# Kernel optimization log

Hardware: AMD Instinct MI355X
Metric: run time of the kernel (lower is better)

## Reference

```python
import jax, jax.numpy as jnp
import numpy as np

ECNUM = 100
CA1NUM = 100
CA3NUM = 100
ACTNUM = 2
TRACKLEN = 100
SIGMA = 5.0
BS = 4096


def setup_inputs() -> dict:
    key = jax.random.key(0)
    ks = jax.random.split(key, 10)
    cue_train = jax.random.randint(ks[0], (BS, TRACKLEN), 0, 3).astype(jnp.int32) - 1  # values in {-1,0,1}
    ec3_last = jax.random.uniform(ks[1], (BS, ECNUM), dtype=jnp.float32)
    ec5_last = jax.random.uniform(ks[2], (BS, ECNUM), dtype=jnp.float32)
    ca1_last = jnp.zeros((BS, CA1NUM), dtype=jnp.float32)
    cueL = (jax.random.uniform(ks[3], (ECNUM,)) < 0.2).astype(jnp.float32)
    cueR = (jax.random.uniform(ks[4], (ECNUM,)) < 0.2).astype(jnp.float32)
    Wec3ca1 = 0.01 * jax.random.uniform(ks[5], (ECNUM, CA1NUM), dtype=jnp.float32)
    Wca3ca1 = 0.01 * jax.random.uniform(ks[6], (CA3NUM, CA1NUM), dtype=jnp.float32)
    Wca1ec5 = 0.01 * jax.random.normal(ks[7], (CA1NUM, ECNUM), dtype=jnp.float32)
    Wca1act = 0.01 * jax.random.uniform(ks[8], (CA1NUM, ACTNUM), dtype=jnp.float32)
    ca1bias = 0.01 * jax.random.uniform(ks[9], (CA1NUM,), dtype=jnp.float32)
    return {
        "bs": BS,
        "cue_train": cue_train,
        "ec3_last": ec3_last,
        "ec5_last": ec5_last,
        "ca1_last": ca1_last,
        "cueL": cueL,
        "cueR": cueR,
        "Wec3ca1": Wec3ca1,
        "Wca3ca1": Wca3ca1,
        "Wca1ec5": Wca1ec5,
        "Wca1act": Wca1act,
        "ca1bias": ca1bias,
    }


def reference(bs, cue_train, ec3_last, ec5_last, ca1_last, cueL, cueR,
              Wec3ca1, Wca3ca1, Wca1ec5, Wca1act, ca1bias):
    # Precompute position-dependent CA3 activity for every timestep: [T, ca3num]
    centers = jnp.linspace(0.0, float(TRACKLEN), CA3NUM)
    xs = jnp.arange(TRACKLEN, dtype=jnp.float32)
    ca3_all = jnp.exp(-(((xs[:, None] - centers[None, :]) / SIGMA) ** 2) / 2.0)
    drive = ca3_all @ Wca3ca1  # [T, ca1num]

    # Sensory input per timestep via conditional gather: [T, bs, ecnum]
    cue_t = cue_train.T[:, :, None]  # [T, bs, 1]
    sensory = jnp.where(cue_t == 1, cueL[None, None, :],
                        jnp.where(cue_t == -1, cueR[None, None, :], 0.0))

    def step(carry, inp):
        ec3, ec5 = carry
        d, s = inp  # d: [ca1num], s: [bs, ecnum]
        ca1 = jax.nn.relu(d[None, :] * (1.0 + jax.nn.sigmoid(ec3 @ Wec3ca1)) - ca1bias)
        ec5 = ec5 + ca1 @ Wca1ec5
        ec5 = 0.69 + 0.3 * jax.nn.sigmoid(4.0 * (ec5 - 0.3))
        ec3 = ec5 * ec3 + s
        return (ec3, ec5), ca1

    (ec3, ec5), ca1his = jax.lax.scan(step, (ec3_last, ec5_last), (drive, sensory))
    ca1 = ca1his[-1]
    actCell = ca1 @ Wca1act
    return actCell, ca1his, ec3, ec5, ca1
```

## Files before the change

### kernel.cpp

```cpp
#include <hip/hip_runtime.h>

#define TLEN 100
#define ECN  100
#define CA1N 100
#define CA3N 100
#define BSZ  4096
#define ACTN 2
#define BT   16

typedef short bf16x8 __attribute__((ext_vector_type(8)));
typedef float f32x4  __attribute__((ext_vector_type(4)));

__device__ __forceinline__ unsigned short f2bf(float f){
  union { float f; unsigned int u; } c; c.f = f;
  return (unsigned short)((c.u + 0x8000u) >> 16);
}
__device__ __forceinline__ float fsigm(float x){
  float e = __expf(-x);
  return __builtin_amdgcn_rcpf(1.0f + e);
}

__global__ void drive_kernel(const float* __restrict__ Wca3ca1, float* __restrict__ drive){
  __shared__ float ca3row[CA3N];
  const int t = blockIdx.x, tid = threadIdx.x;
  if (tid < CA3N){
    float c = (float)tid * (100.0f / 99.0f);
    float d = ((float)t - c) * 0.2f;
    ca3row[tid] = __expf(-0.5f * d * d);
  }
  __syncthreads();
  if (tid < CA1N){
    float acc = 0.f;
    for (int k = 0; k < CA3N; ++k) acc = fmaf(ca3row[k], Wca3ca1[k*CA1N + tid], acc);
    drive[t*CA1N + tid] = acc;
  }
}


__global__ __launch_bounds__(512, 2)
void rnn_kernel(const int*   __restrict__ cue_train,
                const float* __restrict__ ec3_last,
                const float* __restrict__ ec5_last,
                const float* __restrict__ cueL,
                const float* __restrict__ cueR,
                const float* __restrict__ Wec3ca1,
                const float* __restrict__ Wca1ec5,
                const float* __restrict__ Wca1act,
                const float* __restrict__ ca1bias,
                const float* __restrict__ drive,
                float*       __restrict__ out)
{
  __shared__ __align__(16) unsigned short ec3b[4 * 64 * 8];
  __shared__ __align__(16) unsigned short ca1b[4 * 64 * 8];
  __shared__ __align__(16) float ca1f[BT * 132];
  __shared__ signed char cueT[TLEN * BT];

  const int tid = threadIdx.x;
  const int b0  = blockIdx.x * BT;

  float* out_act = out;
  float* out_his = out + (size_t)BSZ * ACTN;
  float* out_e3  = out_his + (size_t)TLEN * BSZ * CA1N;
  float* out_e5  = out_e3 + (size_t)BSZ * ECN;
  float* out_c1  = out_e5 + (size_t)BSZ * ECN;

  for (int idx = tid; idx < 4 * 64 * 8; idx += 512){ ec3b[idx] = 0; ca1b[idx] = 0; }
  for (int idx = tid; idx < BT * TLEN; idx += 512){
    int t = idx >> 4, r = idx & 15;
    cueT[idx] = (signed char)cue_train[(size_t)(b0 + r) * TLEN + t];
  }

  const int lane  = tid & 63;
  const int wv    = tid >> 6;
  const int col16 = lane & 15;
  const int q     = lane >> 4;
  const int col   = wv * 16 + col16;
  const bool okc  = (col < CA1N);
  const bool wactive = (wv < 7);
  const int colc  = okc ? col : 0;

  const int abase = (col >> 5) * 512 + ((col >> 3) & 3) * 128 + (col & 7) + q * 32;

  bf16x8 b1[4], b2[4];
  #pragma unroll
  for (int ks = 0; ks < 4; ++ks){
    #pragma unroll
    for (int jj = 0; jj < 8; ++jj){
      int k = ks * 32 + q * 8 + jj;
      float w1 = 0.f, w2 = 0.f;
      if (k < ECN && okc){
        w1 = Wec3ca1[k * CA1N + col];
        w2 = Wca1ec5[k * ECN  + col];
      }
      b1[ks][jj] = (short)f2bf(w1);
      b2[ks][jj] = (short)f2bf(w2);
    }
  }
  const float bias_c = okc ? ca1bias[col] : 0.f;
  const float cL = okc ? cueL[col] : 0.f;
  const float cR = okc ? cueR[col] : 0.f;

  __syncthreads();

  float ec3v[4], ec5v[4], c1[4] = {0.f,0.f,0.f,0.f};
  #pragma unroll
  for (int i = 0; i < 4; ++i){
    int r = q * 4 + i;
    float v3 = okc ? ec3_last[(size_t)(b0 + r) * ECN + col] : 0.f;
    float v5 = okc ? ec5_last[(size_t)(b0 + r) * ECN + col] : 0.f;
    ec3v[i] = v3; ec5v[i] = v5;
    if (okc) ec3b[abase + i * 8] = f2bf(v3);
  }
  __syncthreads();

  const float* dp = drive + colc;
  float* hp = out_his + (size_t)(b0 + q * 4) * CA1N + colc;

  const bf16x8* fe3 = (const bf16x8*)ec3b;
  const bf16x8* fc1 = (const bf16x8*)ca1b;

  for (int t = 0; t < TLEN; ++t){
    float dv  = *dp; dp += CA1N;
    int   cu4 = *(const int*)(cueT + t * BT + q * 4);

    if (wactive){
      f32x4 aA = {0.f,0.f,0.f,0.f}, aB = {0.f,0.f,0.f,0.f};
      bf16x8 a0 = fe3[  0 + lane];
      bf16x8 a1 = fe3[ 64 + lane];
      bf16x8 a2 = fe3[128 + lane];
      bf16x8 a3 = fe3[192 + lane];
      aA = __builtin_amdgcn_mfma_f32_16x16x32_bf16(a0, b1[0], aA, 0, 0, 0);
      aB = __builtin_amdgcn_mfma_f32_16x16x32_bf16(a1, b1[1], aB, 0, 0, 0);
      aA = __builtin_amdgcn_mfma_f32_16x16x32_bf16(a2, b1[2], aA, 0, 0, 0);
      aB = __builtin_amdgcn_mfma_f32_16x16x32_bf16(a3, b1[3], aB, 0, 0, 0);
      f32x4 z = aA + aB;
      float dmb = dv - bias_c;
      #pragma unroll
      for (int i = 0; i < 4; ++i){
        float v = fmaxf(fmaf(dv, fsigm(z[i]), dmb), 0.f);
        c1[i] = v;
        if (okc) ca1b[abase + i * 8] = f2bf(v);
      }
    }
    __syncthreads();

    if (okc){
      hp[0 * CA1N] = c1[0];
      hp[1 * CA1N] = c1[1];
      hp[2 * CA1N] = c1[2];
      hp[3 * CA1N] = c1[3];
    }
    hp += (size_t)BSZ * CA1N;

    if (wactive){
      f32x4 aA = {0.f,0.f,0.f,0.f}, aB = {0.f,0.f,0.f,0.f};
      bf16x8 a0 = fc1[  0 + lane];
      bf16x8 a1 = fc1[ 64 + lane];
      bf16x8 a2 = fc1[128 + lane];
      bf16x8 a3 = fc1[192 + lane];
      aA = __builtin_amdgcn_mfma_f32_16x16x32_bf16(a0, b2[0], aA, 0, 0, 0);
      aB = __builtin_amdgcn_mfma_f32_16x16x32_bf16(a1, b2[1], aB, 0, 0, 0);
      aA = __builtin_amdgcn_mfma_f32_16x16x32_bf16(a2, b2[2], aA, 0, 0, 0);
      aB = __builtin_amdgcn_mfma_f32_16x16x32_bf16(a3, b2[3], aB, 0, 0, 0);
      f32x4 z2 = aA + aB;
      #pragma unroll
      for (int i = 0; i < 4; ++i){
        float x  = ec5v[i] + z2[i];
        float e5 = fmaf(0.3f, fsigm(fmaf(4.0f, x, -1.2f)), 0.69f);
        ec5v[i] = e5;
        int cu = (cu4 >> (8 * i)) & 0xff;
        float sns = (cu == 1) ? cL : ((cu == 0xff) ? cR : 0.0f);
        float e3 = fmaf(e5, ec3v[i], sns);
        ec3v[i] = e3;
        if (okc) ec3b[abase + i * 8] = f2bf(e3);
      }
    }
    __syncthreads();
  }

  if (okc){
    #pragma unroll
    for (int i = 0; i < 4; ++i){
      int r = q * 4 + i;
      size_t g = (size_t)(b0 + r) * ECN + col;
      out_e3[g] = ec3v[i];
      out_e5[g] = ec5v[i];
      out_c1[g] = c1[i];
      ca1f[r * 132 + col] = c1[i];
    }
  }
  __syncthreads();

  if (tid < BT * ACTN){
    int r = tid >> 1, a = tid & 1;
    float acc = 0.f;
    for (int jj = 0; jj < CA1N; ++jj)
      acc = fmaf(ca1f[r * 132 + jj], Wca1act[jj * ACTN + a], acc);
    out_act[(size_t)(b0 + r) * ACTN + a] = acc;
  }
}

extern "C" void kernel_launch(void* const* d_in, const int* in_sizes, int n_in,
                              void* d_out, int out_size, void* d_ws, size_t ws_size,
                              hipStream_t stream) {
  (void)in_sizes; (void)n_in; (void)out_size; (void)ws_size;
  const int*   cue_train = (const int*)  d_in[1];
  const float* ec3_last  = (const float*)d_in[2];
  const float* ec5_last  = (const float*)d_in[3];
  const float* cueL      = (const float*)d_in[5];
  const float* cueR      = (const float*)d_in[6];
  const float* Wec3ca1   = (const float*)d_in[7];
  const float* Wca3ca1   = (const float*)d_in[8];
  const float* Wca1ec5   = (const float*)d_in[9];
  const float* Wca1act   = (const float*)d_in[10];
  const float* ca1bias   = (const float*)d_in[11];
  float* out   = (float*)d_out;
  float* drive = (float*)d_ws;

  drive_kernel<<<TLEN, 128, 0, stream>>>(Wca3ca1, drive);
  rnn_kernel<<<BSZ / BT, 512, 0, stream>>>(cue_train, ec3_last, ec5_last,
                                           cueL, cueR, Wec3ca1, Wca1ec5,
                                           Wca1act, ca1bias, drive, out);
}
```

Baseline: 289.3 us.

## Halve batch tile per block, stage drive table in LDS, use lightweight barriers

Reduces the batch rows per block from 16 to 8 so twice as many blocks run the serial 100-step recurrence, and raises the occupancy hint to 4 blocks per CU. The MFMA tiles stay 16-row, so half the rows are padding and waste compute. The drive table is copied into shared memory once per block instead of read from global each step. __syncthreads is replaced by an inline waitcnt plus s_barrier to cut barrier overhead. The cost is more LDS per block (about 40KB for the drive table) and redundant MFMA work on the padded rows.

```diff
diff --git a/kernel.cpp b/kernel.cpp
--- a/kernel.cpp
+++ b/kernel.cpp
@@ -6,7 +6,7 @@
 #define CA3N 100
 #define BSZ  4096
 #define ACTN 2
-#define BT   16
+#define BT   8
 
 typedef short bf16x8 __attribute__((ext_vector_type(8)));
 typedef float f32x4  __attribute__((ext_vector_type(4)));
@@ -18,6 +18,9 @@
 __device__ __forceinline__ float fsigm(float x){
   float e = __expf(-x);
   return __builtin_amdgcn_rcpf(1.0f + e);
+}
+__device__ __forceinline__ void lds_barrier(){
+  asm volatile("s_waitcnt lgkmcnt(0)\n\ts_barrier" ::: "memory");
 }
 
 __global__ void drive_kernel(const float* __restrict__ Wca3ca1, float* __restrict__ drive){
@@ -37,7 +40,7 @@
 }
 
 
-__global__ __launch_bounds__(512, 2)
+__global__ __launch_bounds__(512, 4)
 void rnn_kernel(const int*   __restrict__ cue_train,
                 const float* __restrict__ ec3_last,
                 const float* __restrict__ ec5_last,
@@ -50,10 +53,11 @@
                 const float* __restrict__ drive,
                 float*       __restrict__ out)
 {
-  __shared__ __align__(16) unsigned short ec3b[4 * 64 * 8];
-  __shared__ __align__(16) unsigned short ca1b[4 * 64 * 8];
+  __shared__ __align__(16) unsigned short ec3b[2048];
+  __shared__ __align__(16) unsigned short ca1b[2048];
+  __shared__ __align__(16) float driveS[TLEN * CA1N];
   __shared__ __align__(16) float ca1f[BT * 132];
-  __shared__ signed char cueT[TLEN * BT];
+  __shared__ __align__(4)  signed char cueT[TLEN * BT];
 
   const int tid = threadIdx.x;
   const int b0  = blockIdx.x * BT;
@@ -64,10 +68,15 @@
   float* out_e5  = out_e3 + (size_t)BSZ * ECN;
   float* out_c1  = out_e5 + (size_t)BSZ * ECN;
 
-  for (int idx = tid; idx < 4 * 64 * 8; idx += 512){ ec3b[idx] = 0; ca1b[idx] = 0; }
+  for (int idx = tid; idx < 2048; idx += 512){ ec3b[idx] = 0; ca1b[idx] = 0; }
+  {
+    const float4* src = (const float4*)drive;
+    float4*       dst = (float4*)driveS;
+    for (int idx = tid; idx < TLEN * CA1N / 4; idx += 512) dst[idx] = src[idx];
+  }
   for (int idx = tid; idx < BT * TLEN; idx += 512){
-    int t = idx >> 4, r = idx & 15;
-    cueT[idx] = (signed char)cue_train[(size_t)(b0 + r) * TLEN + t];
+    int t = idx >> 3, r = idx & 7;
+    cueT[t * BT + r] = (signed char)cue_train[(size_t)(b0 + r) * TLEN + t];
   }
 
   const int lane  = tid & 63;
@@ -76,6 +85,7 @@
   const int q     = lane >> 4;
   const int col   = wv * 16 + col16;
   const bool okc  = (col < CA1N);
+  const bool rowok = (q < 2);
   const bool wactive = (wv < 7);
   const int colc  = okc ? col : 0;
 
@@ -106,22 +116,22 @@
   #pragma unroll
   for (int i = 0; i < 4; ++i){
     int r = q * 4 + i;
-    float v3 = okc ? ec3_last[(size_t)(b0 + r) * ECN + col] : 0.f;
-    float v5 = okc ? ec5_last[(size_t)(b0 + r) * ECN + col] : 0.f;
+    float v3 = (okc && rowok) ? ec3_last[(size_t)(b0 + r) * ECN + col] : 0.f;
+    float v5 = (okc && rowok) ? ec5_last[(size_t)(b0 + r) * ECN + col] : 0.f;
     ec3v[i] = v3; ec5v[i] = v5;
     if (okc) ec3b[abase + i * 8] = f2bf(v3);
   }
   __syncthreads();
 
-  const float* dp = drive + colc;
-  float* hp = out_his + (size_t)(b0 + q * 4) * CA1N + colc;
+  float* hp = out_his + (size_t)(b0 + (rowok ? q * 4 : 0)) * CA1N + colc;
+  const int cuoff = rowok ? q * 4 : 0;
 
   const bf16x8* fe3 = (const bf16x8*)ec3b;
   const bf16x8* fc1 = (const bf16x8*)ca1b;
 
   for (int t = 0; t < TLEN; ++t){
-    float dv  = *dp; dp += CA1N;
-    int   cu4 = *(const int*)(cueT + t * BT + q * 4);
+    float dv  = driveS[t * CA1N + colc];
+    int   cu4 = *(const int*)(cueT + t * BT + cuoff);
 
     if (wactive){
       f32x4 aA = {0.f,0.f,0.f,0.f}, aB = {0.f,0.f,0.f,0.f};
@@ -142,9 +152,9 @@
         if (okc) ca1b[abase + i * 8] = f2bf(v);
       }
     }
-    __syncthreads();
-
-    if (okc){
+    lds_barrier();
+
+    if (okc && rowok){
       hp[0 * CA1N] = c1[0];
       hp[1 * CA1N] = c1[1];
       hp[2 * CA1N] = c1[2];
@@ -175,10 +185,10 @@
         if (okc) ec3b[abase + i * 8] = f2bf(e3);
       }
     }
-    __syncthreads();
-  }
-
-  if (okc){
+    lds_barrier();
+  }
+
+  if (okc && rowok){
     #pragma unroll
     for (int i = 0; i < 4; ++i){
       int r = q * 4 + i;
```

Measured after the change: 292.2 us. No clear change (+1.0%).
